# Performance work log

Measured on AMD Instinct MI355X. Metric: run time of the kernel, lower is better.

Reference implementation:

```python
import jax, jax.numpy as jnp
import numpy as np

D_MODEL = 1024
NUM_HEADS = 16
D_K = D_MODEL // NUM_HEADS
B, L = 2, 2048


def setup_inputs() -> dict:
    key = jax.random.key(0)
    ks = jax.random.split(key, 10)
    s = 1.0 / np.sqrt(D_MODEL)
    inp = {
        "x": jax.random.normal(ks[0], (B, L, D_MODEL), dtype=jnp.float32),
        "mask": jnp.ones((B, L, L), dtype=jnp.int32),
        "wq": jax.random.uniform(ks[1], (D_MODEL, D_MODEL), jnp.float32, -s, s),
        "bq": jax.random.uniform(ks[2], (D_MODEL,), jnp.float32, -s, s),
        "wk": jax.random.uniform(ks[3], (D_MODEL, D_MODEL), jnp.float32, -s, s),
        "bk": jax.random.uniform(ks[4], (D_MODEL,), jnp.float32, -s, s),
        "wv": jax.random.uniform(ks[5], (D_MODEL, D_MODEL), jnp.float32, -s, s),
        "bv": jax.random.uniform(ks[6], (D_MODEL,), jnp.float32, -s, s),
        "wo": jax.random.uniform(ks[7], (D_MODEL, D_MODEL), jnp.float32, -s, s),
        "bo": jax.random.uniform(ks[8], (D_MODEL,), jnp.float32, -s, s),
    }
    return inp


def reference(x, mask, wq, bq, wk, bk, wv, bv, wo, bo):
    Bs, Ls, C = x.shape
    # linear projections, then split heads: [B, L, C] -> [B, h, L, d_k]
    def split_heads(t):
        return t.reshape(Bs, Ls, NUM_HEADS, D_K).transpose(0, 2, 1, 3)
    q = split_heads(x @ wq + bq)
    k = split_heads(x @ wk + bk)
    v = split_heads(x @ wv + bv)
    scores = jnp.einsum("bhlc,bhkc->bhlk", q, k) / np.sqrt(D_K)
    # mask: [B, L, L] -> [B, 1, L, L]; fill masked positions with -1e9
    scores = jnp.where(mask[:, None, :, :] == 0, jnp.float32(-1e9), scores)
    attn = jax.nn.softmax(scores, axis=-1)  # dropout p=0.0 -> identity
    out = jnp.einsum("bhlk,bhkc->bhlc", attn, v)
    out = out.transpose(0, 2, 1, 3).reshape(Bs, Ls, C)
    return out @ wo + bo
```

## Files before the change

kernel.cpp:

```cpp
#include <hip/hip_runtime.h>
#include <stdint.h>

#define D_MODEL 1024
#define NHEAD   16
#define DK      64
#define BATCH   2
#define SEQ     2048
#define MTOT    (BATCH*SEQ)

typedef unsigned short u16;
typedef unsigned int   u32;
typedef u16    u16x4  __attribute__((ext_vector_type(4)));
typedef u16    u16x8  __attribute__((ext_vector_type(8)));
typedef u32    u32x4  __attribute__((ext_vector_type(4)));
typedef __bf16 bf16x8 __attribute__((ext_vector_type(8)));
typedef float  f32x4  __attribute__((ext_vector_type(4)));
typedef float  f32x16 __attribute__((ext_vector_type(16)));

__device__ __forceinline__ u16 f2bf(float f) {
  union { float f; unsigned u; } v; v.f = f;
  return (u16)((v.u + 0x7fffu + ((v.u >> 16) & 1u)) >> 16);
}

__device__ __forceinline__ void gl_lds16(const void* g, void* l) {
  __builtin_amdgcn_global_load_lds((const __attribute__((address_space(1))) void*)g,
                                   (__attribute__((address_space(3))) void*)l, 16, 0, 0);
}

__device__ __forceinline__ bf16x8 ld_frag(const u16* p) {
  return __builtin_bit_cast(bf16x8, *(const u16x8*)p);
}

__device__ __forceinline__ u32 cvtpk(float lo, float hi) {
  u32 r;
  asm("v_cvt_pk_bf16_f32 %0, %1, %2" : "=v"(r) : "v"(lo), "v"(hi));
  return r;
}

__global__ __launch_bounds__(256) void k_cvt_x(const float* __restrict__ x, u16* __restrict__ xb) {
  int i = blockIdx.x * 256 + threadIdx.x;
  const float4 v = ((const float4*)x)[i];
  u16x4 o; o[0]=f2bf(v.x); o[1]=f2bf(v.y); o[2]=f2bf(v.z); o[3]=f2bf(v.w);
  *(u16x4*)(xb + (size_t)i*4) = o;
}

__global__ __launch_bounds__(256) void k_wtrans(const float* __restrict__ wq, const float* __restrict__ wk,
                                                const float* __restrict__ wv, const float* __restrict__ wo,
                                                u16* __restrict__ wqkv_t, u16* __restrict__ wo_t) {
  __shared__ float tile[32][33];
  const int z = blockIdx.z;
  const float* src = (z==0)?wq:(z==1)?wk:(z==2)?wv:wo;
  const int kb = blockIdx.y*32, nb = blockIdx.x*32;
  const int tx = threadIdx.x & 31, ty = threadIdx.x >> 5;
  #pragma unroll
  for (int i=0;i<4;i++)
    tile[ty + i*8][tx] = src[(size_t)(kb + ty + i*8)*D_MODEL + nb + tx];
  __syncthreads();
  u16* dst = (z<3) ? (wqkv_t + (size_t)z*D_MODEL*D_MODEL) : wo_t;
  #pragma unroll
  for (int i=0;i<4;i++) {
    int n = nb + ty + i*8, k = kb + tx;
    dst[(size_t)n*D_MODEL + k] = f2bf(tile[tx][ty + i*8]);
  }
}

__global__ __launch_bounds__(256) void k_maskpack(const int* __restrict__ mask,
                                                  unsigned long long* __restrict__ mb) {
  const int wid = blockIdx.x*4 + (threadIdx.x >> 6);
  const int lane = threadIdx.x & 63;
  for (int t2 = 0; t2 < 32; ++t2) {
    int word = wid*32 + t2;
    int row = word >> 5;
    int kb = word & 31;
    int m = mask[(size_t)row*SEQ + kb*64 + lane];
    unsigned long long bits = __ballot(m != 0);
    if (lane == 0) mb[word] = bits;
  }
}

__global__ __launch_bounds__(256) void k_vtrans(const u16* __restrict__ V, u16* __restrict__ Vt) {
  __shared__ u16 tile[64][72];
  const int bh = blockIdx.x >> 5;
  const int l0 = (blockIdx.x & 31) * 64;
  const int t = threadIdx.x;
  const u16* src = V + ((size_t)bh*SEQ + l0)*DK;
  #pragma unroll
  for (int j=0;j<2;j++) {
    int idx = t + j*256;
    int r = idx >> 3, c8 = (idx & 7)*8;
    *(u16x8*)&tile[r][c8] = *(const u16x8*)(src + (size_t)r*DK + c8);
  }
  __syncthreads();
  u16* dst = Vt + (size_t)bh*DK*SEQ + l0;
  #pragma unroll
  for (int j=0;j<2;j++) {
    int idx = t + j*256;
    int d = idx >> 3, k8 = (idx & 7)*8;
    u16x8 o;
    #pragma unroll
    for (int e=0;e<8;e++) o[e] = tile[k8 + e][d];
    *(u16x8*)(dst + (size_t)d*SEQ + k8) = o;
  }
}

template<int EPI>
__global__ __launch_bounds__(256) void k_gemm(const u16* __restrict__ A, const u16* __restrict__ Bt,
                                              const int M, const int N, const int K, const int nbm,
                                              const float* __restrict__ bq, const float* __restrict__ bk,
                                              const float* __restrict__ bv,
                                              u16* __restrict__ Qo, u16* __restrict__ Ko, u16* __restrict__ Vo,
                                              const float* __restrict__ bo, float* __restrict__ out) {
  __shared__ u16 As[128*32];
  __shared__ u16 Bs[128*32];
  const int t = threadIdx.x, lane = t & 63, w = t >> 6;
  const int bm = blockIdx.x % nbm, bn = blockIdx.x / nbm;
  const int brow = bm*128, bcol = bn*128;

  const int srow = w*32 + (lane >> 2);
  const int sswz = (lane & 3) ^ ((lane >> 2) & 3);
  const u16* aS0 = A  + (size_t)(brow + srow)*K + sswz*8;
  const u16* aS1 = aS0 + (size_t)16*K;
  const u16* bS0 = Bt + (size_t)(bcol + srow)*K + sswz*8;
  const u16* bS1 = bS0 + (size_t)16*K;
  u16* aD0 = As + w*1024; u16* aD1 = aD0 + 512;
  u16* bD0 = Bs + w*1024; u16* bD1 = bD0 + 512;

  const int wr = w >> 1, wc = w & 1;
  const int slotA = (lane >> 4) ^ (lane & 3);
  const u16* aRd = As + (wr*64 + (lane & 15))*32 + slotA*8;
  const u16* bRd = Bs + (wc*64 + (lane & 15))*32 + slotA*8;

  f32x4 acc[4][4];
  #pragma unroll
  for (int i=0;i<4;i++)
    #pragma unroll
    for (int j=0;j<4;j++) acc[i][j] = (f32x4){0.f,0.f,0.f,0.f};

  for (int kt = 0; kt < K; kt += 32) {
    gl_lds16(aS0 + kt, aD0);
    gl_lds16(aS1 + kt, aD1);
    gl_lds16(bS0 + kt, bD0);
    gl_lds16(bS1 + kt, bD1);
    __syncthreads();
    bf16x8 af[4], bfr[4];
    #pragma unroll
    for (int m=0;m<4;m++) af[m] = ld_frag(aRd + m*512);
    #pragma unroll
    for (int n=0;n<4;n++) bfr[n] = ld_frag(bRd + n*512);
    #pragma unroll
    for (int m=0;m<4;m++)
      #pragma unroll
      for (int n=0;n<4;n++)
        acc[m][n] = __builtin_amdgcn_mfma_f32_16x16x32_bf16(af[m], bfr[n], acc[m][n], 0,0,0);
    __syncthreads();
  }

  const int orow = brow + wr*64 + (lane >> 4)*4;
  const int ocol = bcol + wc*64 + (lane & 15);
  if (EPI == 0) {
    const int mat = ocol >> 10;
    const float* bias = (mat==0) ? bq : (mat==1) ? bk : bv;
    u16* outp = (mat==0) ? Qo : (mat==1) ? Ko : Vo;
    const float scal = (mat==0) ? 0.125f*1.4426950408889634f : 1.0f;
    #pragma unroll
    for (int m=0;m<4;m++) {
      #pragma unroll
      for (int n=0;n<4;n++) {
        int col = ocol + n*16;
        int c = col & 1023;
        float bb = bias[c];
        int h = c >> 6, d = c & 63;
        #pragma unroll
        for (int j=0;j<4;j++) {
          int row = orow + m*16 + j;
          int b = row >> 11, l = row & 2047;
          float v = (acc[m][n][j] + bb) * scal;
          outp[(((size_t)(b*NHEAD + h)*SEQ + l) << 6) + d] = f2bf(v);
        }
      }
    }
  } else {
    #pragma unroll
    for (int m=0;m<4;m++)
      #pragma unroll
      for (int n=0;n<4;n++) {
        int col = ocol + n*16;
        float bb = bo[col];
        #pragma unroll
        for (int j=0;j<4;j++) {
          int row = orow + m*16 + j;
          out[(size_t)row*N + col] = acc[m][n][j] + bb;
        }
      }
  }
}

__global__ __launch_bounds__(512, 4) void k_attn(const u16* __restrict__ Q, const u16* __restrict__ K,
                                                 const u16* __restrict__ Vt,
                                                 const unsigned long long* __restrict__ MB,
                                                 u16* __restrict__ AO) {
  __shared__ char smem[81920];
  const int t = threadIdx.x, lane = t & 63, w = t >> 6;
  const int hf = w >> 2, widx = w & 3;
  const int bid = blockIdx.x;
  const int swz = (bid & 7)*64 + (bid >> 3);
  const int bh = swz >> 4;
  const int q0 = (swz & 15) * 128;
  const int b = bh >> 4, h = bh & 15;
  const int lq = lane & 31, hi = lane >> 5, l7 = lane & 7;

  const int qg = q0 + widx*32 + lq;

  const int sswz = l7 ^ ((lane >> 3) & 7);
  const int srow = widx*16 + (lane >> 3);
  const u16* kSb = K  + ((size_t)bh*SEQ + srow)*DK + sswz*8;
  const u16* vSb = Vt + ((size_t)bh*DK + srow)*SEQ + sswz*8;

  u16* qlds = (u16*)(smem + 65536);
  {
    const int qsrow = w*16 + (lane >> 3);
    const u16* qS = Q + ((size_t)bh*SEQ + q0 + qsrow)*DK + sswz*8;
    gl_lds16(qS, qlds + w*1024);
    gl_lds16(qS + 8*DK, qlds + w*1024 + 512);
  }
  const u16* qrd = qlds + (widx*32 + lq)*64;

  f32x16 o0 = 0.f, o1 = 0.f;
  float m_run = -1e30f, l_run = 0.f;
  const unsigned long long* mbp = MB + ((size_t)b*SEQ + qg)*32;

  #define STAGE(buf, tile) do {                                           \
    const u16* kp_ = kSb + (size_t)(tile)*64*DK;                          \
    const u16* vp_ = vSb + (size_t)(tile)*64;                             \
    u16* kd_ = (u16*)(smem + (buf)*32768 + hf*16384) + widx*1024;         \
    u16* vd_ = (u16*)(smem + (buf)*32768 + hf*16384 + 8192) + widx*1024;  \
    gl_lds16(kp_, kd_); gl_lds16(kp_ + 8*DK, kd_ + 512);                  \
    gl_lds16(vp_, vd_); gl_lds16(vp_ + 8*SEQ, vd_ + 512);                 \
  } while (0)

  STAGE(0, hf*16);
  asm volatile("s_waitcnt vmcnt(0)" ::: "memory");
  __builtin_amdgcn_s_barrier();

  for (int i = 0; i < 16; ++i) {
    const int cur = i & 1;
    if (i + 1 < 16) STAGE(cur ^ 1, hf*16 + i + 1);
    const u16* Kbuf = (const u16*)(smem + cur*32768 + hf*16384);
    const u16* Vbuf = (const u16*)(smem + cur*32768 + hf*16384 + 8192);
    const unsigned long long mb = mbp[hf*16 + i];
    const bool full = __all(mb == ~0ull);

    #pragma unroll
    for (int sub = 0; sub < 2; ++sub) {
      f32x16 s = 0.f;
      __builtin_amdgcn_s_setprio(1);
      #pragma unroll
      for (int ks=0;ks<4;ks++) {
        const int ph = (ks*2 + hi) ^ l7;
        bf16x8 kf = ld_frag(Kbuf + (sub*32 + lq)*64 + ph*8);
        bf16x8 qf = ld_frag(qrd + ph*8);
        s = __builtin_amdgcn_mfma_f32_32x32x16_bf16(kf, qf, s, 0,0,0);
      }
      __builtin_amdgcn_s_setprio(0);

      if (!full) {
        #pragma unroll
        for (int r=0;r<16;r++) {
          int kl = sub*32 + (r&3) + 8*(r>>2) + 4*hi;
          if (!((mb >> kl) & 1ull)) s[r] = -1e9f;
        }
      }

      float tm[8];
      #pragma unroll
      for (int r=0;r<8;r++) tm[r] = fmaxf(s[r], s[8+r]);
      #pragma unroll
      for (int st=4; st>0; st>>=1)
        #pragma unroll
        for (int r=0;r<4;r++) if (r < st) tm[r] = fmaxf(tm[r], tm[r+st]);
      float mx = fmaxf(tm[0], __shfl_xor(tm[0], 32));
      if (!__all(mx <= m_run + 8.0f)) {
        float m_new = fmaxf(m_run, mx);
        float corr = __builtin_amdgcn_exp2f(m_run - m_new);
        l_run *= corr;
        #pragma unroll
        for (int r=0;r<16;r++) { o0[r] *= corr; o1[r] *= corr; }
        m_run = m_new;
      }
      #pragma unroll
      for (int r=0;r<16;r++) s[r] = __builtin_amdgcn_exp2f(s[r] - m_run);
      float ts[8];
      #pragma unroll
      for (int r=0;r<8;r++) ts[r] = s[r] + s[8+r];
      #pragma unroll
      for (int st=4; st>0; st>>=1)
        #pragma unroll
        for (int r=0;r<4;r++) if (r < st) ts[r] += ts[r+st];
      l_run += ts[0] + __shfl_xor(ts[0], 32);

      u32 w0 = cvtpk(s[0],  s[1]),  w1 = cvtpk(s[2],  s[3]);
      u32 w2 = cvtpk(s[4],  s[5]),  w3 = cvtpk(s[6],  s[7]);
      u32 w4 = cvtpk(s[8],  s[9]),  w5 = cvtpk(s[10], s[11]);
      u32 w6 = cvtpk(s[12], s[13]), w7 = cvtpk(s[14], s[15]);
      asm volatile("v_permlane32_swap_b32 %0, %1" : "+v"(w0), "+v"(w2));
      asm volatile("v_permlane32_swap_b32 %0, %1" : "+v"(w1), "+v"(w3));
      asm volatile("v_permlane32_swap_b32 %0, %1" : "+v"(w4), "+v"(w6));
      asm volatile("v_permlane32_swap_b32 %0, %1" : "+v"(w5), "+v"(w7));
      bf16x8 pa0 = __builtin_bit_cast(bf16x8, (u32x4){w0, w1, w2, w3});
      bf16x8 pa1 = __builtin_bit_cast(bf16x8, (u32x4){w4, w5, w6, w7});
      const int ph0 = ((sub*2+0)*2 + hi) ^ l7;
      const int ph1 = ((sub*2+1)*2 + hi) ^ l7;
      {
        bf16x8 v00 = ld_frag(Vbuf + lq*64 + ph0*8);
        bf16x8 v01 = ld_frag(Vbuf + lq*64 + ph1*8);
        __builtin_amdgcn_s_setprio(1);
        o0 = __builtin_amdgcn_mfma_f32_32x32x16_bf16(v00, pa0, o0, 0,0,0);
        o0 = __builtin_amdgcn_mfma_f32_32x32x16_bf16(v01, pa1, o0, 0,0,0);
        __builtin_amdgcn_s_setprio(0);
      }
      {
        bf16x8 v10 = ld_frag(Vbuf + (32+lq)*64 + ph0*8);
        bf16x8 v11 = ld_frag(Vbuf + (32+lq)*64 + ph1*8);
        __builtin_amdgcn_s_setprio(1);
        o1 = __builtin_amdgcn_mfma_f32_32x32x16_bf16(v10, pa0, o1, 0,0,0);
        o1 = __builtin_amdgcn_mfma_f32_32x32x16_bf16(v11, pa1, o1, 0,0,0);
        __builtin_amdgcn_s_setprio(0);
      }
    }

    asm volatile("s_waitcnt vmcnt(0)" ::: "memory");
    __builtin_amdgcn_s_barrier();
  }
  #undef STAGE

  float* marea = (float*)smem;
  if (hf == 1) {
    float* p = marea + (size_t)(widx*64 + lane)*35;
    #pragma unroll
    for (int r=0;r<16;r++) { p[r] = o0[r]; p[16+r] = o1[r]; }
    p[32] = m_run; p[33] = l_run;
  }
  __syncthreads();
  if (hf == 0) {
    const float* p = marea + (size_t)(widx*64 + lane)*35;
    float m1 = p[32], l1 = p[33];
    float mm = fmaxf(m_run, m1);
    float c0 = __builtin_amdgcn_exp2f(m_run - mm);
    float c1 = __builtin_amdgcn_exp2f(m1 - mm);
    float inv = 1.0f / (l_run*c0 + l1*c1);
    size_t base = ((size_t)(b*SEQ + qg))*D_MODEL + h*DK;
    u16x4 g;
    #pragma unroll
    for (int rr=0;rr<4;rr++) {
      #pragma unroll
      for (int i2=0;i2<4;i2++) g[i2] = f2bf((o0[rr*4+i2]*c0 + p[rr*4+i2]*c1) * inv);
      *(u16x4*)(AO + base + rr*8 + hi*4) = g;
    }
    #pragma unroll
    for (int rr=0;rr<4;rr++) {
      #pragma unroll
      for (int i2=0;i2<4;i2++) g[i2] = f2bf((o1[rr*4+i2]*c0 + p[16+rr*4+i2]*c1) * inv);
      *(u16x4*)(AO + base + 32 + rr*8 + hi*4) = g;
    }
  }
}

extern "C" void kernel_launch(void* const* d_in, const int* in_sizes, int n_in,
                              void* d_out, int out_size, void* d_ws, size_t ws_size,
                              hipStream_t stream) {
  const float* x  = (const float*)d_in[0];
  const int*  msk = (const int*)d_in[1];
  const float* wq = (const float*)d_in[2];
  const float* bq = (const float*)d_in[3];
  const float* wk = (const float*)d_in[4];
  const float* bk = (const float*)d_in[5];
  const float* wv = (const float*)d_in[6];
  const float* bv = (const float*)d_in[7];
  const float* wo = (const float*)d_in[8];
  const float* bo = (const float*)d_in[9];
  float* out = (float*)d_out;

  char* ws = (char*)d_ws;
  size_t off = 0;
  u16* Xb   = (u16*)(ws + off); off += (size_t)MTOT*D_MODEL*2;
  u16* Wqkv = (u16*)(ws + off); off += (size_t)3*D_MODEL*D_MODEL*2;
  u16* Wot  = (u16*)(ws + off); off += (size_t)D_MODEL*D_MODEL*2;
  u16* Qb   = (u16*)(ws + off); off += (size_t)BATCH*NHEAD*SEQ*DK*2;
  u16* Kb   = (u16*)(ws + off); off += (size_t)BATCH*NHEAD*SEQ*DK*2;
  u16* Vb   = (u16*)(ws + off); off += (size_t)BATCH*NHEAD*SEQ*DK*2;
  u16* Vtb  = (u16*)(ws + off); off += (size_t)BATCH*NHEAD*SEQ*DK*2;
  u16* AO   = (u16*)(ws + off); off += (size_t)MTOT*D_MODEL*2;
  unsigned long long* Mb = (unsigned long long*)(ws + off);

  k_cvt_x<<<MTOT*D_MODEL/4/256, 256, 0, stream>>>(x, Xb);
  k_wtrans<<<dim3(32,32,4), 256, 0, stream>>>(wq, wk, wv, wo, Wqkv, Wot);
  k_maskpack<<<1024, 256, 0, stream>>>(msk, Mb);
  k_gemm<0><<<(MTOT/128)*(3*D_MODEL/128), 256, 0, stream>>>(
      Xb, Wqkv, MTOT, 3*D_MODEL, D_MODEL, MTOT/128,
      bq, bk, bv, Qb, Kb, Vb, nullptr, nullptr);
  k_vtrans<<<BATCH*NHEAD*(SEQ/64), 256, 0, stream>>>(Vb, Vtb);
  k_attn<<<BATCH*NHEAD*(SEQ/128), 512, 0, stream>>>(Qb, Kb, Vtb, Mb, AO);
  k_gemm<1><<<(MTOT/128)*(D_MODEL/128), 256, 0, stream>>>(
      AO, Wot, MTOT, D_MODEL, D_MODEL, MTOT/128,
      nullptr, nullptr, nullptr, nullptr, nullptr, nullptr, bo, out);
}
```

Before: 148.8 us.

## Fuse prep kernels, swizzle GEMM block order, compute softmax row sums via MFMA

Merges the x conversion, weight transpose and mask-packing kernels into a single launch, which removes two kernel launch gaps. Remaps GEMM block indices across 8 groups, likely to spread work across XCDs and improve L2 locality. In attention, the row-sum of the softmax numerator now comes from extra MFMAs against a ones vector instead of a shuffle-based reduction, and the max reduction becomes a linear chain. This trades VALU and shuffle work for two more matrix instructions per sub-tile, and the row sum is now taken from the bf16-rounded probabilities.

```diff
diff --git a/kernel.cpp b/kernel.cpp
--- a/kernel.cpp
+++ b/kernel.cpp
@@ -37,44 +37,46 @@
   return r;
 }
 
-__global__ __launch_bounds__(256) void k_cvt_x(const float* __restrict__ x, u16* __restrict__ xb) {
-  int i = blockIdx.x * 256 + threadIdx.x;
-  const float4 v = ((const float4*)x)[i];
-  u16x4 o; o[0]=f2bf(v.x); o[1]=f2bf(v.y); o[2]=f2bf(v.z); o[3]=f2bf(v.w);
-  *(u16x4*)(xb + (size_t)i*4) = o;
-}
-
-__global__ __launch_bounds__(256) void k_wtrans(const float* __restrict__ wq, const float* __restrict__ wk,
-                                                const float* __restrict__ wv, const float* __restrict__ wo,
-                                                u16* __restrict__ wqkv_t, u16* __restrict__ wo_t) {
-  __shared__ float tile[32][33];
-  const int z = blockIdx.z;
-  const float* src = (z==0)?wq:(z==1)?wk:(z==2)?wv:wo;
-  const int kb = blockIdx.y*32, nb = blockIdx.x*32;
-  const int tx = threadIdx.x & 31, ty = threadIdx.x >> 5;
-  #pragma unroll
-  for (int i=0;i<4;i++)
-    tile[ty + i*8][tx] = src[(size_t)(kb + ty + i*8)*D_MODEL + nb + tx];
-  __syncthreads();
-  u16* dst = (z<3) ? (wqkv_t + (size_t)z*D_MODEL*D_MODEL) : wo_t;
-  #pragma unroll
-  for (int i=0;i<4;i++) {
-    int n = nb + ty + i*8, k = kb + tx;
-    dst[(size_t)n*D_MODEL + k] = f2bf(tile[tx][ty + i*8]);
-  }
-}
-
-__global__ __launch_bounds__(256) void k_maskpack(const int* __restrict__ mask,
-                                                  unsigned long long* __restrict__ mb) {
-  const int wid = blockIdx.x*4 + (threadIdx.x >> 6);
-  const int lane = threadIdx.x & 63;
-  for (int t2 = 0; t2 < 32; ++t2) {
-    int word = wid*32 + t2;
-    int row = word >> 5;
-    int kb = word & 31;
-    int m = mask[(size_t)row*SEQ + kb*64 + lane];
-    unsigned long long bits = __ballot(m != 0);
-    if (lane == 0) mb[word] = bits;
+__global__ __launch_bounds__(256) void k_prep(const float* __restrict__ x, u16* __restrict__ xb,
+                                              const float* __restrict__ wq, const float* __restrict__ wk,
+                                              const float* __restrict__ wv, const float* __restrict__ wo,
+                                              u16* __restrict__ wqkv_t, u16* __restrict__ wo_t,
+                                              const int* __restrict__ mask,
+                                              unsigned long long* __restrict__ mb) {
+  const int bid = blockIdx.x;
+  if (bid < 4096) {
+    int i = bid * 256 + threadIdx.x;
+    const float4 v = ((const float4*)x)[i];
+    u16x4 o; o[0]=f2bf(v.x); o[1]=f2bf(v.y); o[2]=f2bf(v.z); o[3]=f2bf(v.w);
+    *(u16x4*)(xb + (size_t)i*4) = o;
+  } else if (bid < 8192) {
+    __shared__ float tile[32][33];
+    const int idx = bid - 4096;
+    const int z = idx >> 10;
+    const float* src = (z==0)?wq:(z==1)?wk:(z==2)?wv:wo;
+    const int kb = ((idx >> 5) & 31)*32, nb = (idx & 31)*32;
+    const int tx = threadIdx.x & 31, ty = threadIdx.x >> 5;
+    #pragma unroll
+    for (int i=0;i<4;i++)
+      tile[ty + i*8][tx] = src[(size_t)(kb + ty + i*8)*D_MODEL + nb + tx];
+    __syncthreads();
+    u16* dst = (z<3) ? (wqkv_t + (size_t)z*D_MODEL*D_MODEL) : wo_t;
+    #pragma unroll
+    for (int i=0;i<4;i++) {
+      int n = nb + ty + i*8, k = kb + tx;
+      dst[(size_t)n*D_MODEL + k] = f2bf(tile[tx][ty + i*8]);
+    }
+  } else {
+    const int wid = (bid - 8192)*4 + (threadIdx.x >> 6);
+    const int lane = threadIdx.x & 63;
+    for (int t2 = 0; t2 < 32; ++t2) {
+      int word = wid*32 + t2;
+      int row = word >> 5;
+      int kb = word & 31;
+      int m = mask[(size_t)row*SEQ + kb*64 + lane];
+      unsigned long long bits = __ballot(m != 0);
+      if (lane == 0) mb[word] = bits;
+    }
   }
 }
 
@@ -113,7 +115,9 @@
   __shared__ u16 As[128*32];
   __shared__ u16 Bs[128*32];
   const int t = threadIdx.x, lane = t & 63, w = t >> 6;
-  const int bm = blockIdx.x % nbm, bn = blockIdx.x / nbm;
+  const int cpx = gridDim.x >> 3;
+  const int bswz = (blockIdx.x & 7)*cpx + (blockIdx.x >> 3);
+  const int bm = bswz % nbm, bn = bswz / nbm;
   const int brow = bm*128, bcol = bn*128;
 
   const int srow = w*32 + (lane >> 2);
@@ -225,8 +229,13 @@
   }
   const u16* qrd = qlds + (widx*32 + lq)*64;
 
-  f32x16 o0 = 0.f, o1 = 0.f;
-  float m_run = -1e30f, l_run = 0.f;
+  u16x8 ones8;
+  #pragma unroll
+  for (int i=0;i<8;i++) ones8[i] = 0x3F80;
+  const bf16x8 ones = __builtin_bit_cast(bf16x8, ones8);
+
+  f32x16 o0 = 0.f, o1 = 0.f, lacc = 0.f;
+  float m_run = -1e30f;
   const unsigned long long* mbp = MB + ((size_t)b*SEQ + qg)*32;
 
   #define STAGE(buf, tile) do {                                           \
@@ -271,32 +280,20 @@
         }
       }
 
-      float tm[8];
-      #pragma unroll
-      for (int r=0;r<8;r++) tm[r] = fmaxf(s[r], s[8+r]);
-      #pragma unroll
-      for (int st=4; st>0; st>>=1)
-        #pragma unroll
-        for (int r=0;r<4;r++) if (r < st) tm[r] = fmaxf(tm[r], tm[r+st]);
-      float mx = fmaxf(tm[0], __shfl_xor(tm[0], 32));
+      float mx = fmaxf(s[0], s[1]);
+      #pragma unroll
+      for (int r=2;r<16;r++) mx = fmaxf(mx, s[r]);
+      mx = fmaxf(mx, __shfl_xor(mx, 32));
       if (!__all(mx <= m_run + 8.0f)) {
         float m_new = fmaxf(m_run, mx);
         float corr = __builtin_amdgcn_exp2f(m_run - m_new);
-        l_run *= corr;
+        lacc[0] *= corr;
         #pragma unroll
         for (int r=0;r<16;r++) { o0[r] *= corr; o1[r] *= corr; }
         m_run = m_new;
       }
       #pragma unroll
       for (int r=0;r<16;r++) s[r] = __builtin_amdgcn_exp2f(s[r] - m_run);
-      float ts[8];
-      #pragma unroll
-      for (int r=0;r<8;r++) ts[r] = s[r] + s[8+r];
-      #pragma unroll
-      for (int st=4; st>0; st>>=1)
-        #pragma unroll
-        for (int r=0;r<4;r++) if (r < st) ts[r] += ts[r+st];
-      l_run += ts[0] + __shfl_xor(ts[0], 32);
 
       u32 w0 = cvtpk(s[0],  s[1]),  w1 = cvtpk(s[2],  s[3]);
       u32 w2 = cvtpk(s[4],  s[5]),  w3 = cvtpk(s[6],  s[7]);
@@ -324,6 +321,8 @@
         __builtin_amdgcn_s_setprio(1);
         o1 = __builtin_amdgcn_mfma_f32_32x32x16_bf16(v10, pa0, o1, 0,0,0);
         o1 = __builtin_amdgcn_mfma_f32_32x32x16_bf16(v11, pa1, o1, 0,0,0);
+        lacc = __builtin_amdgcn_mfma_f32_32x32x16_bf16(ones, pa0, lacc, 0,0,0);
+        lacc = __builtin_amdgcn_mfma_f32_32x32x16_bf16(ones, pa1, lacc, 0,0,0);
         __builtin_amdgcn_s_setprio(0);
       }
     }
@@ -333,6 +332,7 @@
   }
   #undef STAGE
 
+  const float l_run = lacc[0];
   float* marea = (float*)smem;
   if (hf == 1) {
     float* p = marea + (size_t)(widx*64 + lane)*35;
@@ -392,9 +392,7 @@
   u16* AO   = (u16*)(ws + off); off += (size_t)MTOT*D_MODEL*2;
   unsigned long long* Mb = (unsigned long long*)(ws + off);
 
-  k_cvt_x<<<MTOT*D_MODEL/4/256, 256, 0, stream>>>(x, Xb);
-  k_wtrans<<<dim3(32,32,4), 256, 0, stream>>>(wq, wk, wv, wo, Wqkv, Wot);
-  k_maskpack<<<1024, 256, 0, stream>>>(msk, Mb);
+  k_prep<<<9216, 256, 0, stream>>>(x, Xb, wq, wk, wv, wo, Wqkv, Wot, msk, Mb);
   k_gemm<0><<<(MTOT/128)*(3*D_MODEL/128), 256, 0, stream>>>(
       Xb, Wqkv, MTOT, 3*D_MODEL, D_MODEL, MTOT/128,
       bq, bk, bv, Qb, Kb, Vb, nullptr, nullptr);
```

Result: no change. 148.3 us (-0.3%).

## Fuse prep kernels, write V transposed from GEMM, add full-mask bitmap, swizzle GEMM blocks

Applied to the files above, without the earlier changes.

Merges the x conversion, weight transpose and mask packing into one launch. The QKV GEMM epilogue now writes V directly in transposed layout, so the separate V transpose kernel and its buffer are gone. Mask packing also emits a per-row 32-bit bitmap of fully unmasked key tiles, and attention reads it once so the 64-bit mask word is only loaded for partial tiles. GEMM block indices are remapped in groups of 8 to change the cache access pattern. The transposed V stores are 8-byte writes strided by the sequence length, which may coalesce less well than the old row-major writes.

```diff
diff --git a/kernel.cpp b/kernel.cpp
--- a/kernel.cpp
+++ b/kernel.cpp
@@ -37,69 +37,48 @@
   return r;
 }
 
-__global__ __launch_bounds__(256) void k_cvt_x(const float* __restrict__ x, u16* __restrict__ xb) {
-  int i = blockIdx.x * 256 + threadIdx.x;
-  const float4 v = ((const float4*)x)[i];
-  u16x4 o; o[0]=f2bf(v.x); o[1]=f2bf(v.y); o[2]=f2bf(v.z); o[3]=f2bf(v.w);
-  *(u16x4*)(xb + (size_t)i*4) = o;
-}
-
-__global__ __launch_bounds__(256) void k_wtrans(const float* __restrict__ wq, const float* __restrict__ wk,
-                                                const float* __restrict__ wv, const float* __restrict__ wo,
-                                                u16* __restrict__ wqkv_t, u16* __restrict__ wo_t) {
-  __shared__ float tile[32][33];
-  const int z = blockIdx.z;
-  const float* src = (z==0)?wq:(z==1)?wk:(z==2)?wv:wo;
-  const int kb = blockIdx.y*32, nb = blockIdx.x*32;
-  const int tx = threadIdx.x & 31, ty = threadIdx.x >> 5;
-  #pragma unroll
-  for (int i=0;i<4;i++)
-    tile[ty + i*8][tx] = src[(size_t)(kb + ty + i*8)*D_MODEL + nb + tx];
-  __syncthreads();
-  u16* dst = (z<3) ? (wqkv_t + (size_t)z*D_MODEL*D_MODEL) : wo_t;
-  #pragma unroll
-  for (int i=0;i<4;i++) {
-    int n = nb + ty + i*8, k = kb + tx;
-    dst[(size_t)n*D_MODEL + k] = f2bf(tile[tx][ty + i*8]);
-  }
-}
-
-__global__ __launch_bounds__(256) void k_maskpack(const int* __restrict__ mask,
-                                                  unsigned long long* __restrict__ mb) {
-  const int wid = blockIdx.x*4 + (threadIdx.x >> 6);
-  const int lane = threadIdx.x & 63;
-  for (int t2 = 0; t2 < 32; ++t2) {
-    int word = wid*32 + t2;
-    int row = word >> 5;
-    int kb = word & 31;
-    int m = mask[(size_t)row*SEQ + kb*64 + lane];
-    unsigned long long bits = __ballot(m != 0);
-    if (lane == 0) mb[word] = bits;
-  }
-}
-
-__global__ __launch_bounds__(256) void k_vtrans(const u16* __restrict__ V, u16* __restrict__ Vt) {
-  __shared__ u16 tile[64][72];
-  const int bh = blockIdx.x >> 5;
-  const int l0 = (blockIdx.x & 31) * 64;
-  const int t = threadIdx.x;
-  const u16* src = V + ((size_t)bh*SEQ + l0)*DK;
-  #pragma unroll
-  for (int j=0;j<2;j++) {
-    int idx = t + j*256;
-    int r = idx >> 3, c8 = (idx & 7)*8;
-    *(u16x8*)&tile[r][c8] = *(const u16x8*)(src + (size_t)r*DK + c8);
-  }
-  __syncthreads();
-  u16* dst = Vt + (size_t)bh*DK*SEQ + l0;
-  #pragma unroll
-  for (int j=0;j<2;j++) {
-    int idx = t + j*256;
-    int d = idx >> 3, k8 = (idx & 7)*8;
-    u16x8 o;
-    #pragma unroll
-    for (int e=0;e<8;e++) o[e] = tile[k8 + e][d];
-    *(u16x8*)(dst + (size_t)d*SEQ + k8) = o;
+__global__ __launch_bounds__(256) void k_prep(const float* __restrict__ x, u16* __restrict__ xb,
+                                              const float* __restrict__ wq, const float* __restrict__ wk,
+                                              const float* __restrict__ wv, const float* __restrict__ wo,
+                                              u16* __restrict__ wqkv_t, u16* __restrict__ wo_t,
+                                              const int* __restrict__ mask,
+                                              unsigned long long* __restrict__ mb,
+                                              u32* __restrict__ fullm) {
+  const int bid = blockIdx.x;
+  if (bid < 4096) {
+    int i = bid * 256 + threadIdx.x;
+    const float4 v = ((const float4*)x)[i];
+    u16x4 o; o[0]=f2bf(v.x); o[1]=f2bf(v.y); o[2]=f2bf(v.z); o[3]=f2bf(v.w);
+    *(u16x4*)(xb + (size_t)i*4) = o;
+  } else if (bid < 8192) {
+    __shared__ float tile[32][33];
+    const int idx = bid - 4096;
+    const int z = idx >> 10;
+    const float* src = (z==0)?wq:(z==1)?wk:(z==2)?wv:wo;
+    const int kb = ((idx >> 5) & 31)*32, nb = (idx & 31)*32;
+    const int tx = threadIdx.x & 31, ty = threadIdx.x >> 5;
+    #pragma unroll
+    for (int i=0;i<4;i++)
+      tile[ty + i*8][tx] = src[(size_t)(kb + ty + i*8)*D_MODEL + nb + tx];
+    __syncthreads();
+    u16* dst = (z<3) ? (wqkv_t + (size_t)z*D_MODEL*D_MODEL) : wo_t;
+    #pragma unroll
+    for (int i=0;i<4;i++) {
+      int n = nb + ty + i*8, k = kb + tx;
+      dst[(size_t)n*D_MODEL + k] = f2bf(tile[tx][ty + i*8]);
+    }
+  } else {
+    const int wid = (bid - 8192)*4 + (threadIdx.x >> 6);
+    const int lane = threadIdx.x & 63;
+    u32 fmacc = 0;
+    for (int t2 = 0; t2 < 32; ++t2) {
+      int word = wid*32 + t2;
+      int m = mask[(size_t)wid*SEQ + t2*64 + lane];
+      unsigned long long bits = __ballot(m != 0);
+      if (bits == ~0ull) fmacc |= (1u << t2);
+      if (lane == 0) mb[word] = bits;
+    }
+    if (lane == 0) fullm[wid] = fmacc;
   }
 }
 
@@ -113,7 +92,9 @@
   __shared__ u16 As[128*32];
   __shared__ u16 Bs[128*32];
   const int t = threadIdx.x, lane = t & 63, w = t >> 6;
-  const int bm = blockIdx.x % nbm, bn = blockIdx.x / nbm;
+  const int cpx = gridDim.x >> 3;
+  const int bswz = (blockIdx.x & 7)*cpx + (blockIdx.x >> 3);
+  const int bm = bswz % nbm, bn = bswz / nbm;
   const int brow = bm*128, bcol = bn*128;
 
   const int srow = w*32 + (lane >> 2);
@@ -159,23 +140,41 @@
   const int ocol = bcol + wc*64 + (lane & 15);
   if (EPI == 0) {
     const int mat = ocol >> 10;
-    const float* bias = (mat==0) ? bq : (mat==1) ? bk : bv;
-    u16* outp = (mat==0) ? Qo : (mat==1) ? Ko : Vo;
-    const float scal = (mat==0) ? 0.125f*1.4426950408889634f : 1.0f;
-    #pragma unroll
-    for (int m=0;m<4;m++) {
-      #pragma unroll
-      for (int n=0;n<4;n++) {
-        int col = ocol + n*16;
-        int c = col & 1023;
-        float bb = bias[c];
-        int h = c >> 6, d = c & 63;
-        #pragma unroll
-        for (int j=0;j<4;j++) {
-          int row = orow + m*16 + j;
-          int b = row >> 11, l = row & 2047;
-          float v = (acc[m][n][j] + bb) * scal;
-          outp[(((size_t)(b*NHEAD + h)*SEQ + l) << 6) + d] = f2bf(v);
+    if (mat == 2) {
+      #pragma unroll
+      for (int m=0;m<4;m++) {
+        const int row0 = orow + m*16;
+        const int b = row0 >> 11, l = row0 & 2047;
+        #pragma unroll
+        for (int n=0;n<4;n++) {
+          const int c = (ocol + n*16) & 1023;
+          const float bb = bv[c];
+          const int h = c >> 6, d = c & 63;
+          u16x4 g;
+          #pragma unroll
+          for (int j=0;j<4;j++) g[j] = f2bf(acc[m][n][j] + bb);
+          *(u16x4*)(Vo + ((size_t)((b*NHEAD + h)*DK + d))*SEQ + l) = g;
+        }
+      }
+    } else {
+      const float* bias = (mat==0) ? bq : bk;
+      u16* outp = (mat==0) ? Qo : Ko;
+      const float scal = (mat==0) ? 0.125f*1.4426950408889634f : 1.0f;
+      #pragma unroll
+      for (int m=0;m<4;m++) {
+        #pragma unroll
+        for (int n=0;n<4;n++) {
+          int col = ocol + n*16;
+          int c = col & 1023;
+          float bb = bias[c];
+          int h = c >> 6, d = c & 63;
+          #pragma unroll
+          for (int j=0;j<4;j++) {
+            int row = orow + m*16 + j;
+            int b = row >> 11, l = row & 2047;
+            float v = (acc[m][n][j] + bb) * scal;
+            outp[(((size_t)(b*NHEAD + h)*SEQ + l) << 6) + d] = f2bf(v);
+          }
         }
       }
     }
@@ -198,6 +197,7 @@
 __global__ __launch_bounds__(512, 4) void k_attn(const u16* __restrict__ Q, const u16* __restrict__ K,
                                                  const u16* __restrict__ Vt,
                                                  const unsigned long long* __restrict__ MB,
+                                                 const u32* __restrict__ FM,
                                                  u16* __restrict__ AO) {
   __shared__ char smem[81920];
   const int t = threadIdx.x, lane = t & 63, w = t >> 6;
@@ -225,9 +225,10 @@
   }
   const u16* qrd = qlds + (widx*32 + lq)*64;
 
+  const u32 fm = FM[(size_t)b*SEQ + qg];
+
   f32x16 o0 = 0.f, o1 = 0.f;
   float m_run = -1e30f, l_run = 0.f;
-  const unsigned long long* mbp = MB + ((size_t)b*SEQ + qg)*32;
 
   #define STAGE(buf, tile) do {                                           \
     const u16* kp_ = kSb + (size_t)(tile)*64*DK;                          \
@@ -247,8 +248,10 @@
     if (i + 1 < 16) STAGE(cur ^ 1, hf*16 + i + 1);
     const u16* Kbuf = (const u16*)(smem + cur*32768 + hf*16384);
     const u16* Vbuf = (const u16*)(smem + cur*32768 + hf*16384 + 8192);
-    const unsigned long long mb = mbp[hf*16 + i];
-    const bool full = __all(mb == ~0ull);
+    const int ktg = hf*16 + i;
+    const bool full = __all((fm >> ktg) & 1u);
+    unsigned long long mb = ~0ull;
+    if (!full) mb = MB[((size_t)b*SEQ + qg)*32 + ktg];
 
     #pragma unroll
     for (int sub = 0; sub < 2; ++sub) {
@@ -387,19 +390,16 @@
   u16* Wot  = (u16*)(ws + off); off += (size_t)D_MODEL*D_MODEL*2;
   u16* Qb   = (u16*)(ws + off); off += (size_t)BATCH*NHEAD*SEQ*DK*2;
   u16* Kb   = (u16*)(ws + off); off += (size_t)BATCH*NHEAD*SEQ*DK*2;
-  u16* Vb   = (u16*)(ws + off); off += (size_t)BATCH*NHEAD*SEQ*DK*2;
   u16* Vtb  = (u16*)(ws + off); off += (size_t)BATCH*NHEAD*SEQ*DK*2;
   u16* AO   = (u16*)(ws + off); off += (size_t)MTOT*D_MODEL*2;
-  unsigned long long* Mb = (unsigned long long*)(ws + off);
-
-  k_cvt_x<<<MTOT*D_MODEL/4/256, 256, 0, stream>>>(x, Xb);
-  k_wtrans<<<dim3(32,32,4), 256, 0, stream>>>(wq, wk, wv, wo, Wqkv, Wot);
-  k_maskpack<<<1024, 256, 0, stream>>>(msk, Mb);
+  unsigned long long* Mb = (unsigned long long*)(ws + off); off += (size_t)MTOT*32*8;
+  u32* FM   = (u32*)(ws + off); off += (size_t)MTOT*4;
+
+  k_prep<<<9216, 256, 0, stream>>>(x, Xb, wq, wk, wv, wo, Wqkv, Wot, msk, Mb, FM);
   k_gemm<0><<<(MTOT/128)*(3*D_MODEL/128), 256, 0, stream>>>(
       Xb, Wqkv, MTOT, 3*D_MODEL, D_MODEL, MTOT/128,
-      bq, bk, bv, Qb, Kb, Vb, nullptr, nullptr);
-  k_vtrans<<<BATCH*NHEAD*(SEQ/64), 256, 0, stream>>>(Vb, Vtb);
-  k_attn<<<BATCH*NHEAD*(SEQ/128), 512, 0, stream>>>(Qb, Kb, Vtb, Mb, AO);
+      bq, bk, bv, Qb, Kb, Vtb, nullptr, nullptr);
+  k_attn<<<BATCH*NHEAD*(SEQ/128), 512, 0, stream>>>(Qb, Kb, Vtb, Mb, FM, AO);
   k_gemm<1><<<(MTOT/128)*(D_MODEL/128), 256, 0, stream>>>(
       AO, Wot, MTOT, D_MODEL, D_MODEL, MTOT/128,
       nullptr, nullptr, nullptr, nullptr, nullptr, nullptr, bo, out);
```

Measured after the change: 159.1 us. +6.9%, slower.
